# Kernel optimization log

Measured on AMD Instinct MI355X. Metric: run time of the kernel, lower is better.

The kernel has to match this reference:

```python
import jax, jax.numpy as jnp
import numpy as np

E, MAX_M, K, N = 8, 2048, 2048, 8192

def setup_inputs() -> dict:
    key = jax.random.key(0)
    k1, k2, k3 = jax.random.split(key, 3)
    x_padded = jax.random.normal(k1, (E, MAX_M, K), dtype=jnp.float32)
    stacked_weights = jax.random.normal(k2, (E, N, K), dtype=jnp.float32) * 0.02
    m_sizes = jax.random.randint(k3, (E,), 0, MAX_M, dtype=jnp.int32)
    return {"x_padded": x_padded, "stacked_weights": stacked_weights, "m_sizes": m_sizes}

def reference(x_padded, stacked_weights, m_sizes):
    # valid-token mask per expert: [E, MAX_M]
    mask = (jnp.arange(MAX_M, dtype=jnp.int32)[None, :] < m_sizes[:, None])
    # zero padded rows (pad_expert_inputs fills with zeros)
    x = jnp.where(mask[:, :, None], x_padded, jnp.zeros((), x_padded.dtype))
    # grouped GEMM via batched matmul: [E, M, K] x [E, N, K]^T -> [E, M, N]
    out = jnp.einsum('emk,enk->emn', x, stacked_weights)
    # rows beyond m_sizes[i] are sliced away in the original; mask them to zero
    return jnp.where(mask[:, :, None], out, jnp.zeros((), out.dtype))
```

## Files before the change

kernel.cpp:

```cpp
#include <hip/hip_runtime.h>
#include <hip/hip_bf16.h>


#define NE   8
#define MAXM 2048
#define KD   2048
#define ND   8192

#define BM   256
#define BN   256
#define BK   64
#define NTS  (KD/BK)

typedef __attribute__((ext_vector_type(8))) short          short8;
typedef __attribute__((ext_vector_type(8))) unsigned short us8;
typedef __attribute__((ext_vector_type(4))) float          f32x4;
typedef __attribute__((ext_vector_type(4))) unsigned short us4;

__device__ __forceinline__ unsigned short f2bf(float f) {
    union { float f; unsigned u; } v; v.f = f;
    unsigned u = v.u;
    return (unsigned short)((u + 0x7FFFu + ((u >> 16) & 1u)) >> 16);
}

__device__ __forceinline__ void gload16(const void* g, void* l) {
    __builtin_amdgcn_global_load_lds(
        (const __attribute__((address_space(1))) void*)g,
        (__attribute__((address_space(3))) void*)l, 16, 0, 0);
}

__global__ __launch_bounds__(256) void cvt_all_kernel(const float* __restrict__ x,
                                                      const float* __restrict__ w,
                                                      unsigned short* __restrict__ xb,
                                                      unsigned short* __restrict__ wb,
                                                      const int* __restrict__ ms) {
    int b = blockIdx.x;
    int t = threadIdx.x;
    if (b < NE * MAXM) {
        int e = b >> 11, m = b & 2047;
        if (m >= ms[e]) return;
        const float* s = x + ((size_t)e * MAXM + m) * KD;
        unsigned short* d = xb + ((size_t)e * MAXM + m) * KD;
        const f32x4* s4 = (const f32x4*)(s + t * 8);
        f32x4 a = s4[0], bb = s4[1];
        us8 v = (us8){f2bf(a[0]), f2bf(a[1]), f2bf(a[2]), f2bf(a[3]),
                      f2bf(bb[0]), f2bf(bb[1]), f2bf(bb[2]), f2bf(bb[3])};
        *(us8*)(d + t * 8) = v;
    } else {
        const int nW8 = (int)(((size_t)NE * ND * KD) / 8);
        int i = (b - NE * MAXM) * 256 + t;
        int stride = 2048 * 256;
        for (; i < nW8; i += stride) {
            const f32x4* s = (const f32x4*)(w + (size_t)i * 8);
            f32x4 a = s[0], bb = s[1];
            us8 v = (us8){f2bf(a[0]), f2bf(a[1]), f2bf(a[2]), f2bf(a[3]),
                          f2bf(bb[0]), f2bf(bb[1]), f2bf(bb[2]), f2bf(bb[3])};
            *(us8*)(wb + (size_t)i * 8) = v;
        }
    }
}

__global__ __launch_bounds__(512, 2) void ggemm_pers(
    const unsigned short* __restrict__ xb,
    const unsigned short* __restrict__ wb,
    const int*   __restrict__ ms,
    float*       __restrict__ out)
{
    int p   = blockIdx.x;
    int xcd = p & 7;
    int jj  = p >> 3;
    int tid = threadIdx.x;

    __shared__ int s_live[8], s_dead[8], s_cnt[2];
    __shared__ unsigned short Ak[2][2][BM * 32];
    __shared__ unsigned short Bk[2][2][BN * 32];

    if (tid == 0) {
        int nl = 0, nd = 0, cumL = 0, cumD = 0, il = jj, id = jj;
        #pragma unroll
        for (int e = 0; e < NE; ++e) {
            int L = (ms[e] + 255) >> 8;
            int cntL = L << 2, cntD = (8 - L) << 2;
            while (il < cumL + cntL) { int o = il - cumL; s_live[nl++] = (e << 5) | ((o >> 2) << 2) | (o & 3); il += 32; }
            while (id < cumD + cntD) { int o = id - cumD; s_dead[nd++] = (e << 5) | ((L + (o >> 2)) << 2) | (o & 3); id += 32; }
            cumL += cntL; cumD += cntD;
        }
        s_cnt[0] = nl; s_cnt[1] = nd;
    }
    __syncthreads();

    int ndead = s_cnt[1];
    #pragma unroll 1
    for (int d = 0; d < ndead; ++d) {
        int v = s_dead[d]; int e = v >> 5, br = (v >> 2) & 7, bcl = v & 3;
        float* outE = out + (size_t)e * MAXM * ND;
        int row0 = br * BM, col0 = (xcd * 4 + bcl) * BN;
        f32x4 z = (f32x4){0.f, 0.f, 0.f, 0.f};
        #pragma unroll
        for (int q = 0; q < 32; ++q) {
            int i2 = tid + q * 512;
            int rr = i2 >> 6, cc = (i2 & 63) << 2;
            *(f32x4*)(outE + (size_t)(row0 + rr) * ND + col0 + cc) = z;
        }
    }
    int nlive = s_cnt[0];
    if (nlive == 0) return;

    int wid = tid >> 6, lane = tid & 63;
    int wr = wid >> 2, wc = wid & 3;
    int lr = lane & 15, kg = lane >> 4;
    int srow = lane >> 2;
    int ss   = (lane & 3) ^ ((lane >> 3) & 3);

    auto stageA = [&](int b, int kh, const unsigned short* xP, int kt) {
        #pragma unroll
        for (int q = 0; q < 2; ++q) {
            int blk = wid * 2 + q;
            const unsigned short* src =
                xP + (size_t)(blk * 16 + srow) * KD + kt * BK + kh * 32 + ss * 8;
            gload16(src, (char*)&Ak[b][kh][0] + blk * 1024);
        }
    };
    auto stageB = [&](int b, int kh, const unsigned short* wP, int kt) {
        #pragma unroll
        for (int q = 0; q < 2; ++q) {
            int blk = wid * 2 + q;
            const unsigned short* src =
                wP + (size_t)(blk * 16 + srow) * KD + kt * BK + kh * 32 + ss * 8;
            gload16(src, (char*)&Bk[b][kh][0] + blk * 1024);
        }
    };
    auto ldA = [&](short8* a, int b, int kh) {
        #pragma unroll
        for (int mf = 0; mf < 8; ++mf) {
            int row  = wr * 128 + mf * 16 + lr;
            int slot = kg ^ ((row >> 1) & 3);
            a[mf] = *(const short8*)&Ak[b][kh][row * 32 + slot * 8];
        }
    };
    auto ldB4 = [&](short8* bf, int b, int kh) {
        #pragma unroll
        for (int i = 0; i < 4; ++i) {
            int row  = wc * 64 + i * 16 + lr;
            int slot = kg ^ ((row >> 1) & 3);
            bf[i] = *(const short8*)&Bk[b][kh][row * 32 + slot * 8];
        }
    };

    f32x4 acc[8][4];
    #pragma unroll
    for (int mf = 0; mf < 8; ++mf)
        #pragma unroll
        for (int nf = 0; nf < 4; ++nf)
            acc[mf][nf] = (f32x4){0.f, 0.f, 0.f, 0.f};

    const unsigned short *xC, *wC, *xN, *wN;
    float *oC, *oN;
    int msC, r0C, c0C, msN, r0N, c0N;
    {
        int v = s_live[0]; int e = v >> 5, br = (v >> 2) & 7, bcl = v & 3;
        r0C = br * BM; c0C = (xcd * 4 + bcl) * BN; msC = ms[e];
        xC = xb + ((size_t)e * MAXM + r0C) * KD;
        wC = wb + ((size_t)e * ND + c0C) * KD;
        oC = out + (size_t)e * MAXM * ND;
    }
    if (nlive > 1) {
        int v = s_live[1]; int e = v >> 5, br = (v >> 2) & 7, bcl = v & 3;
        r0N = br * BM; c0N = (xcd * 4 + bcl) * BN; msN = ms[e];
        xN = xb + ((size_t)e * MAXM + r0N) * KD;
        wN = wb + ((size_t)e * ND + c0N) * KD;
        oN = out + (size_t)e * MAXM * ND;
    } else { xN = xC; wN = wC; oN = oC; msN = msC; r0N = r0C; c0N = c0C; }

    stageA(0, 0, xC, 0); stageB(0, 0, wC, 0);
    stageA(0, 1, xC, 0); stageB(0, 1, wC, 0);
    stageA(1, 0, xC, 1); stageB(1, 0, wC, 1);
    asm volatile("s_waitcnt vmcnt(8)" ::: "memory");
    __builtin_amdgcn_s_barrier();

    #pragma unroll 1
    for (int s = 0; s < nlive; ++s) {
        bool last  = (s + 1 >= nlive);
        bool alive = (r0C + wr * 128) < msC;

        auto tile = [&](int b, int kt) {
            bool g1 = (kt + 1 < NTS) || (!last);
            bool g2 = (kt + 2 < NTS) || (!last);
            const unsigned short* xS1 = (kt + 1 < NTS) ? xC : xN;
            const unsigned short* wS1 = (kt + 1 < NTS) ? wC : wN;
            int k1 = (kt + 1 < NTS) ? kt + 1 : 0;
            const unsigned short* xS2 = (kt + 2 < NTS) ? xC : xN;
            const unsigned short* wS2 = (kt + 2 < NTS) ? wC : wN;
            int k2 = (kt + 2 < NTS) ? kt + 2 : kt + 2 - NTS;

            short8 a[8], bf[4];
            if (alive) { ldA(a, b, 0); ldB4(bf, b, 0); }
            if (g1) { stageA(b ^ 1, 1, xS1, k1); stageB(b ^ 1, 1, wS1, k1); }
            __builtin_amdgcn_s_barrier();
            __builtin_amdgcn_s_setprio(1);
            if (alive) {
                #pragma unroll
                for (int mf = 0; mf < 8; ++mf)
                    #pragma unroll
                    for (int nf = 0; nf < 4; ++nf)
                        acc[mf][nf] = __builtin_amdgcn_mfma_f32_16x16x32_bf16(a[mf], bf[nf], acc[mf][nf], 0, 0, 0);
            }
            __builtin_amdgcn_s_setprio(0);
            if (g1) { asm volatile("s_waitcnt vmcnt(8)" ::: "memory"); }
            else    { asm volatile("s_waitcnt vmcnt(0)" ::: "memory"); }
            __builtin_amdgcn_s_barrier();
            if (alive) { ldA(a, b, 1); ldB4(bf, b, 1); }
            if (g2) { stageA(b, 0, xS2, k2); stageB(b, 0, wS2, k2); }
            __builtin_amdgcn_s_barrier();
            __builtin_amdgcn_s_setprio(1);
            if (alive) {
                #pragma unroll
                for (int mf = 0; mf < 8; ++mf)
                    #pragma unroll
                    for (int nf = 0; nf < 4; ++nf)
                        acc[mf][nf] = __builtin_amdgcn_mfma_f32_16x16x32_bf16(a[mf], bf[nf], acc[mf][nf], 0, 0, 0);
            }
            __builtin_amdgcn_s_setprio(0);
            if (g2) { asm volatile("s_waitcnt vmcnt(8)" ::: "memory"); }
            else    { asm volatile("s_waitcnt vmcnt(0)" ::: "memory"); }
            __builtin_amdgcn_s_barrier();
        };

        #pragma unroll 1
        for (int kt = 0; kt < NTS; kt += 2) {
            tile(0, kt);
            tile(1, kt + 1);
        }

        #pragma unroll
        for (int mf = 0; mf < 8; ++mf) {
            int rbase = r0C + wr * 128 + mf * 16 + kg * 4;
            #pragma unroll
            for (int nf = 0; nf < 4; ++nf) {
                int gc = c0C + wc * 64 + nf * 16 + lr;
                #pragma unroll
                for (int q = 0; q < 4; ++q) {
                    int gr = rbase + q;
                    float v = (gr < msC) ? acc[mf][nf][q] : 0.f;
                    oC[(size_t)gr * ND + gc] = v;
                    acc[mf][nf][q] = 0.f;
                }
            }
        }

        xC = xN; wC = wN; oC = oN; msC = msN; r0C = r0N; c0C = c0N;
        if (s + 2 < nlive) {
            int v = s_live[s + 2]; int e = v >> 5, br = (v >> 2) & 7, bcl = v & 3;
            r0N = br * BM; c0N = (xcd * 4 + bcl) * BN; msN = ms[e];
            xN = xb + ((size_t)e * MAXM + r0N) * KD;
            wN = wb + ((size_t)e * ND + c0N) * KD;
            oN = out + (size_t)e * MAXM * ND;
        }
    }
}

#define FBM 128
#define FBK 32
#define FTM (MAXM/FBM)
#define FTN (ND/FBM)
#define FNT (KD/FBK)
#define LSTR 40
__global__ __launch_bounds__(256, 2) void ggemm_fused(
    const float* __restrict__ x, const float* __restrict__ w,
    const int* __restrict__ ms, float* __restrict__ out)
{
    int nwg  = gridDim.x;
    int orig = blockIdx.x;
    int cpx  = nwg >> 3;
    int bid  = (orig & 7) * cpx + (orig >> 3);
    int e   = bid / (FTM * FTN);
    int rem = bid % (FTM * FTN);
    int br  = rem % FTM;
    int bc  = rem / FTM;
    int m_size = ms[e];
    int row0 = br * FBM, col0 = bc * FBM;
    float* outE = out + (size_t)e * MAXM * ND;
    int tid = threadIdx.x;

    if (row0 >= m_size) {
        f32x4 z = (f32x4){0.f, 0.f, 0.f, 0.f};
        #pragma unroll
        for (int q = 0; q < 16; ++q) {
            int i2 = tid + q * 256;
            int rr = i2 >> 5, cc = (i2 & 31) << 2;
            *(f32x4*)(outE + (size_t)(row0 + rr) * ND + col0 + cc) = z;
        }
        return;
    }

    const float* xE = x + ((size_t)e * MAXM + row0) * KD;
    const float* wE = w + ((size_t)e * ND   + col0) * KD;

    __shared__ unsigned short As[2][FBM][LSTR];
    __shared__ unsigned short Bs[2][FBM][LSTR];

    int sr  = tid >> 3;
    int sc4 = tid & 7;
    int wid = tid >> 6, lane = tid & 63;
    int wr = wid >> 1, wc = wid & 1;
    int lr = lane & 15, kg = lane >> 4;

    f32x4 acc[4][4];
    #pragma unroll
    for (int m = 0; m < 4; ++m)
        #pragma unroll
        for (int n = 0; n < 4; ++n)
            acc[m][n] = (f32x4){0.f, 0.f, 0.f, 0.f};

    {
        #pragma unroll
        for (int q = 0; q < 4; ++q) {
            int r0 = sr + q * 32;
            f32x4 av = *(const f32x4*)(xE + (size_t)r0 * KD + sc4 * 4);
            f32x4 bv = *(const f32x4*)(wE + (size_t)r0 * KD + sc4 * 4);
            us4 ah = (us4){f2bf(av[0]), f2bf(av[1]), f2bf(av[2]), f2bf(av[3])};
            us4 bh = (us4){f2bf(bv[0]), f2bf(bv[1]), f2bf(bv[2]), f2bf(bv[3])};
            *(us4*)&As[0][r0][sc4 * 4] = ah;
            *(us4*)&Bs[0][r0][sc4 * 4] = bh;
        }
    }
    __syncthreads();

    for (int t = 0; t < FNT; ++t) {
        int cur = t & 1;
        f32x4 av[4], bv[4];
        bool pre = (t + 1 < FNT);
        if (pre) {
            const float* xk = xE + (size_t)(t + 1) * FBK;
            const float* wk = wE + (size_t)(t + 1) * FBK;
            #pragma unroll
            for (int q = 0; q < 4; ++q) {
                int r0 = sr + q * 32;
                av[q] = *(const f32x4*)(xk + (size_t)r0 * KD + sc4 * 4);
                bv[q] = *(const f32x4*)(wk + (size_t)r0 * KD + sc4 * 4);
            }
        }
        short8 a[4], b[4];
        #pragma unroll
        for (int m = 0; m < 4; ++m)
            a[m] = *(const short8*)&As[cur][wr * 64 + m * 16 + lr][kg * 8];
        #pragma unroll
        for (int n = 0; n < 4; ++n)
            b[n] = *(const short8*)&Bs[cur][wc * 64 + n * 16 + lr][kg * 8];
        #pragma unroll
        for (int m = 0; m < 4; ++m)
            #pragma unroll
            for (int n = 0; n < 4; ++n)
                acc[m][n] = __builtin_amdgcn_mfma_f32_16x16x32_bf16(a[m], b[n], acc[m][n], 0, 0, 0);

        if (pre) {
            int nb = cur ^ 1;
            #pragma unroll
            for (int q = 0; q < 4; ++q) {
                int r0 = sr + q * 32;
                us4 ah = (us4){f2bf(av[q][0]), f2bf(av[q][1]), f2bf(av[q][2]), f2bf(av[q][3])};
                us4 bh = (us4){f2bf(bv[q][0]), f2bf(bv[q][1]), f2bf(bv[q][2]), f2bf(bv[q][3])};
                *(us4*)&As[nb][r0][sc4 * 4] = ah;
                *(us4*)&Bs[nb][r0][sc4 * 4] = bh;
            }
        }
        __syncthreads();
    }

    #pragma unroll
    for (int m = 0; m < 4; ++m) {
        int rbase = row0 + wr * 64 + m * 16 + kg * 4;
        #pragma unroll
        for (int n = 0; n < 4; ++n) {
            int gc = col0 + wc * 64 + n * 16 + lr;
            #pragma unroll
            for (int q = 0; q < 4; ++q) {
                int gr = rbase + q;
                float v = (gr < m_size) ? acc[m][n][q] : 0.f;
                outE[(size_t)gr * ND + gc] = v;
            }
        }
    }
}

extern "C" void kernel_launch(void* const* d_in, const int* in_sizes, int n_in,
                              void* d_out, int out_size, void* d_ws, size_t ws_size,
                              hipStream_t stream) {
    const float* x  = (const float*)d_in[0];
    const float* w  = (const float*)d_in[1];
    const int*   ms = (const int*)d_in[2];
    float* out = (float*)d_out;

    const size_t xElems = (size_t)NE * MAXM * KD;
    const size_t wElems = (size_t)NE * ND   * KD;
    const size_t need   = (xElems + wElems) * 2;

    if (ws_size >= need) {
        unsigned short* xb = (unsigned short*)d_ws;
        unsigned short* wb = xb + xElems;
        cvt_all_kernel<<<NE * MAXM + 2048, 256, 0, stream>>>(x, w, xb, wb, ms);
        ggemm_pers<<<256, 512, 0, stream>>>(xb, wb, ms, out);
    } else {
        ggemm_fused<<<dim3(NE * (MAXM/FBM) * (ND/FBM)), dim3(256), 0, stream>>>(x, w, ms, out);
    }
}
```

Measured before the change: 581.1 us.

## Shrink persistent GEMM tiles to 128x256 with 3-stage BK=32 pipeline

Reworks the persistent bf16 GEMM from 256x256 tiles with 512 threads to 128x256 tiles with 256 threads and 512 persistent blocks. The K loop goes from two half-stages over BK=64 to a triple-buffered ring over BK=32, and the schedule switches to 128-row granularity. Finer row granularity wastes less work on partially filled expert tiles and drops the per-wave alive check, but each tile reuses less data, needs more loads per flop, and runs more barriers.

```diff
diff --git a/kernel.cpp b/kernel.cpp
--- a/kernel.cpp
+++ b/kernel.cpp
@@ -7,9 +7,9 @@
 #define KD   2048
 #define ND   8192
 
-#define BM   256
+#define BM   128
 #define BN   256
-#define BK   64
+#define BK   32
 #define NTS  (KD/BK)
 
 typedef __attribute__((ext_vector_type(8))) short          short8;
@@ -60,7 +60,7 @@
     }
 }
 
-__global__ __launch_bounds__(512, 2) void ggemm_pers(
+__global__ __launch_bounds__(256, 2) void ggemm_pers(
     const unsigned short* __restrict__ xb,
     const unsigned short* __restrict__ wb,
     const int*   __restrict__ ms,
@@ -72,17 +72,17 @@
     int tid = threadIdx.x;
 
     __shared__ int s_live[8], s_dead[8], s_cnt[2];
-    __shared__ unsigned short Ak[2][2][BM * 32];
-    __shared__ unsigned short Bk[2][2][BN * 32];
+    __shared__ unsigned short Ak[3][BM * 32];
+    __shared__ unsigned short Bk[3][BN * 32];
 
     if (tid == 0) {
         int nl = 0, nd = 0, cumL = 0, cumD = 0, il = jj, id = jj;
         #pragma unroll
         for (int e = 0; e < NE; ++e) {
-            int L = (ms[e] + 255) >> 8;
-            int cntL = L << 2, cntD = (8 - L) << 2;
-            while (il < cumL + cntL) { int o = il - cumL; s_live[nl++] = (e << 5) | ((o >> 2) << 2) | (o & 3); il += 32; }
-            while (id < cumD + cntD) { int o = id - cumD; s_dead[nd++] = (e << 5) | ((L + (o >> 2)) << 2) | (o & 3); id += 32; }
+            int L = (ms[e] + 127) >> 7;
+            int cntL = L << 2, cntD = (16 - L) << 2;
+            while (il < cumL + cntL) { int o = il - cumL; s_live[nl++] = (e << 6) | ((o >> 2) << 2) | (o & 3); il += 64; }
+            while (id < cumD + cntD) { int o = id - cumD; s_dead[nd++] = (e << 6) | (((L + (o >> 2))) << 2) | (o & 3); id += 64; }
             cumL += cntL; cumD += cntD;
         }
         s_cnt[0] = nl; s_cnt[1] = nd;
@@ -92,13 +92,13 @@
     int ndead = s_cnt[1];
     #pragma unroll 1
     for (int d = 0; d < ndead; ++d) {
-        int v = s_dead[d]; int e = v >> 5, br = (v >> 2) & 7, bcl = v & 3;
+        int v = s_dead[d]; int e = v >> 6, br = (v >> 2) & 15, bcl = v & 3;
         float* outE = out + (size_t)e * MAXM * ND;
         int row0 = br * BM, col0 = (xcd * 4 + bcl) * BN;
         f32x4 z = (f32x4){0.f, 0.f, 0.f, 0.f};
         #pragma unroll
         for (int q = 0; q < 32; ++q) {
-            int i2 = tid + q * 512;
+            int i2 = tid + q * 256;
             int rr = i2 >> 6, cc = (i2 & 63) << 2;
             *(f32x4*)(outE + (size_t)(row0 + rr) * ND + col0 + cc) = z;
         }
@@ -107,43 +107,43 @@
     if (nlive == 0) return;
 
     int wid = tid >> 6, lane = tid & 63;
-    int wr = wid >> 2, wc = wid & 3;
+    int wc = wid;
     int lr = lane & 15, kg = lane >> 4;
     int srow = lane >> 2;
     int ss   = (lane & 3) ^ ((lane >> 3) & 3);
 
-    auto stageA = [&](int b, int kh, const unsigned short* xP, int kt) {
+    auto stageA = [&](int r, const unsigned short* xP, int kt) {
         #pragma unroll
         for (int q = 0; q < 2; ++q) {
             int blk = wid * 2 + q;
             const unsigned short* src =
-                xP + (size_t)(blk * 16 + srow) * KD + kt * BK + kh * 32 + ss * 8;
-            gload16(src, (char*)&Ak[b][kh][0] + blk * 1024);
+                xP + (size_t)(blk * 16 + srow) * KD + kt * BK + ss * 8;
+            gload16(src, (char*)&Ak[r][0] + blk * 1024);
         }
     };
-    auto stageB = [&](int b, int kh, const unsigned short* wP, int kt) {
-        #pragma unroll
-        for (int q = 0; q < 2; ++q) {
-            int blk = wid * 2 + q;
+    auto stageB = [&](int r, const unsigned short* wP, int kt) {
+        #pragma unroll
+        for (int q = 0; q < 4; ++q) {
+            int blk = wid * 4 + q;
             const unsigned short* src =
-                wP + (size_t)(blk * 16 + srow) * KD + kt * BK + kh * 32 + ss * 8;
-            gload16(src, (char*)&Bk[b][kh][0] + blk * 1024);
+                wP + (size_t)(blk * 16 + srow) * KD + kt * BK + ss * 8;
+            gload16(src, (char*)&Bk[r][0] + blk * 1024);
         }
     };
-    auto ldA = [&](short8* a, int b, int kh) {
+    auto ldA = [&](short8* a, int r) {
         #pragma unroll
         for (int mf = 0; mf < 8; ++mf) {
-            int row  = wr * 128 + mf * 16 + lr;
+            int row  = mf * 16 + lr;
             int slot = kg ^ ((row >> 1) & 3);
-            a[mf] = *(const short8*)&Ak[b][kh][row * 32 + slot * 8];
+            a[mf] = *(const short8*)&Ak[r][row * 32 + slot * 8];
         }
     };
-    auto ldB4 = [&](short8* bf, int b, int kh) {
+    auto ldB4 = [&](short8* bf, int r) {
         #pragma unroll
         for (int i = 0; i < 4; ++i) {
             int row  = wc * 64 + i * 16 + lr;
             int slot = kg ^ ((row >> 1) & 3);
-            bf[i] = *(const short8*)&Bk[b][kh][row * 32 + slot * 8];
+            bf[i] = *(const short8*)&Bk[r][row * 32 + slot * 8];
         }
     };
 
@@ -158,83 +158,59 @@
     float *oC, *oN;
     int msC, r0C, c0C, msN, r0N, c0N;
     {
-        int v = s_live[0]; int e = v >> 5, br = (v >> 2) & 7, bcl = v & 3;
+        int v = s_live[0]; int e = v >> 6, br = (v >> 2) & 15, bcl = v & 3;
         r0C = br * BM; c0C = (xcd * 4 + bcl) * BN; msC = ms[e];
         xC = xb + ((size_t)e * MAXM + r0C) * KD;
         wC = wb + ((size_t)e * ND + c0C) * KD;
         oC = out + (size_t)e * MAXM * ND;
     }
     if (nlive > 1) {
-        int v = s_live[1]; int e = v >> 5, br = (v >> 2) & 7, bcl = v & 3;
+        int v = s_live[1]; int e = v >> 6, br = (v >> 2) & 15, bcl = v & 3;
         r0N = br * BM; c0N = (xcd * 4 + bcl) * BN; msN = ms[e];
         xN = xb + ((size_t)e * MAXM + r0N) * KD;
         wN = wb + ((size_t)e * ND + c0N) * KD;
         oN = out + (size_t)e * MAXM * ND;
     } else { xN = xC; wN = wC; oN = oC; msN = msC; r0N = r0C; c0N = c0C; }
 
-    stageA(0, 0, xC, 0); stageB(0, 0, wC, 0);
-    stageA(0, 1, xC, 0); stageB(0, 1, wC, 0);
-    stageA(1, 0, xC, 1); stageB(1, 0, wC, 1);
-    asm volatile("s_waitcnt vmcnt(8)" ::: "memory");
+    stageA(0, xC, 0); stageB(0, wC, 0);
+    stageA(1, xC, 1); stageB(1, wC, 1);
+    asm volatile("s_waitcnt vmcnt(6)" ::: "memory");
     __builtin_amdgcn_s_barrier();
+
+    int cur = 0;
 
     #pragma unroll 1
     for (int s = 0; s < nlive; ++s) {
-        bool last  = (s + 1 >= nlive);
-        bool alive = (r0C + wr * 128) < msC;
-
-        auto tile = [&](int b, int kt) {
-            bool g1 = (kt + 1 < NTS) || (!last);
-            bool g2 = (kt + 2 < NTS) || (!last);
-            const unsigned short* xS1 = (kt + 1 < NTS) ? xC : xN;
-            const unsigned short* wS1 = (kt + 1 < NTS) ? wC : wN;
-            int k1 = (kt + 1 < NTS) ? kt + 1 : 0;
-            const unsigned short* xS2 = (kt + 2 < NTS) ? xC : xN;
-            const unsigned short* wS2 = (kt + 2 < NTS) ? wC : wN;
+        bool last = (s + 1 >= nlive);
+
+        #pragma unroll 1
+        for (int kt = 0; kt < NTS; ++kt) {
+            bool stg = (kt + 2 < NTS) || (!last);
+            const unsigned short* xS = (kt + 2 < NTS) ? xC : xN;
+            const unsigned short* wS = (kt + 2 < NTS) ? wC : wN;
             int k2 = (kt + 2 < NTS) ? kt + 2 : kt + 2 - NTS;
-
+            int rs = (cur >= 1) ? cur - 1 : 2;
+
+            if (stg) { stageA(rs, xS, k2); stageB(rs, wS, k2); }
             short8 a[8], bf[4];
-            if (alive) { ldA(a, b, 0); ldB4(bf, b, 0); }
-            if (g1) { stageA(b ^ 1, 1, xS1, k1); stageB(b ^ 1, 1, wS1, k1); }
+            ldB4(bf, cur); ldA(a, cur);
             __builtin_amdgcn_s_barrier();
             __builtin_amdgcn_s_setprio(1);
-            if (alive) {
+            #pragma unroll
+            for (int mf = 0; mf < 8; ++mf)
                 #pragma unroll
-                for (int mf = 0; mf < 8; ++mf)
-                    #pragma unroll
-                    for (int nf = 0; nf < 4; ++nf)
-                        acc[mf][nf] = __builtin_amdgcn_mfma_f32_16x16x32_bf16(a[mf], bf[nf], acc[mf][nf], 0, 0, 0);
-            }
+                for (int nf = 0; nf < 4; ++nf)
+                    acc[mf][nf] = __builtin_amdgcn_mfma_f32_16x16x32_bf16(a[mf], bf[nf], acc[mf][nf], 0, 0, 0);
             __builtin_amdgcn_s_setprio(0);
-            if (g1) { asm volatile("s_waitcnt vmcnt(8)" ::: "memory"); }
-            else    { asm volatile("s_waitcnt vmcnt(0)" ::: "memory"); }
+            if (stg) { asm volatile("s_waitcnt vmcnt(6)" ::: "memory"); }
+            else     { asm volatile("s_waitcnt vmcnt(0)" ::: "memory"); }
             __builtin_amdgcn_s_barrier();
-            if (alive) { ldA(a, b, 1); ldB4(bf, b, 1); }
-            if (g2) { stageA(b, 0, xS2, k2); stageB(b, 0, wS2, k2); }
-            __builtin_amdgcn_s_barrier();
-            __builtin_amdgcn_s_setprio(1);
-            if (alive) {
-                #pragma unroll
-                for (int mf = 0; mf < 8; ++mf)
-                    #pragma unroll
-                    for (int nf = 0; nf < 4; ++nf)
-                        acc[mf][nf] = __builtin_amdgcn_mfma_f32_16x16x32_bf16(a[mf], bf[nf], acc[mf][nf], 0, 0, 0);
-            }
-            __builtin_amdgcn_s_setprio(0);
-            if (g2) { asm volatile("s_waitcnt vmcnt(8)" ::: "memory"); }
-            else    { asm volatile("s_waitcnt vmcnt(0)" ::: "memory"); }
-            __builtin_amdgcn_s_barrier();
-        };
-
-        #pragma unroll 1
-        for (int kt = 0; kt < NTS; kt += 2) {
-            tile(0, kt);
-            tile(1, kt + 1);
+            cur = (cur + 1 == 3) ? 0 : cur + 1;
         }
 
         #pragma unroll
         for (int mf = 0; mf < 8; ++mf) {
-            int rbase = r0C + wr * 128 + mf * 16 + kg * 4;
+            int rbase = r0C + mf * 16 + kg * 4;
             #pragma unroll
             for (int nf = 0; nf < 4; ++nf) {
                 int gc = c0C + wc * 64 + nf * 16 + lr;
@@ -250,7 +226,7 @@
 
         xC = xN; wC = wN; oC = oN; msC = msN; r0C = r0N; c0C = c0N;
         if (s + 2 < nlive) {
-            int v = s_live[s + 2]; int e = v >> 5, br = (v >> 2) & 7, bcl = v & 3;
+            int v = s_live[s + 2]; int e = v >> 6, br = (v >> 2) & 15, bcl = v & 3;
             r0N = br * BM; c0N = (xcd * 4 + bcl) * BN; msN = ms[e];
             xN = xb + ((size_t)e * MAXM + r0N) * KD;
             wN = wb + ((size_t)e * ND + c0N) * KD;
@@ -399,7 +375,7 @@
         unsigned short* xb = (unsigned short*)d_ws;
         unsigned short* wb = xb + xElems;
         cvt_all_kernel<<<NE * MAXM + 2048, 256, 0, stream>>>(x, w, xb, wb, ms);
-        ggemm_pers<<<256, 512, 0, stream>>>(xb, wb, ms, out);
+        ggemm_pers<<<512, 256, 0, stream>>>(xb, wb, ms, out);
     } else {
         ggemm_fused<<<dim3(NE * (MAXM/FBM) * (ND/FBM)), dim3(256), 0, stream>>>(x, w, ms, out);
     }
```

Measured after the change: 588.0 us. No clear change (+1.2%).
